# Performance work log

Measured on AMD Instinct MI355X. Metric: run time of the kernel, lower is better.

## Reference

```python
import jax, jax.numpy as jnp
import numpy as np

T = 4096          # total packed tokens (4 docs x 1024)
NUM_DOCS = 4
H = 16            # n_heads
D = 64            # head_dim == v_head_dim
TOPK = 64         # per-token top-k KV selection (<= min doc len)


def setup_inputs() -> dict:
    key = jax.random.key(0)
    kq, kk, kv, ki, ks = jax.random.split(key, 5)
    q = jax.random.normal(kq, (T, H, D), dtype=jnp.float32)
    k = jax.random.normal(kk, (T, H, D), dtype=jnp.float32)
    v = jax.random.normal(kv, (T, H, D), dtype=jnp.float32)
    # 4 equal-length documents of 1024 tokens
    cu_seqlens = (jnp.arange(NUM_DOCS + 1, dtype=jnp.int32) * (T // NUM_DOCS))
    # global top-k indices; reference clamps them into the owning document
    topk_indices = jax.random.randint(ki, (T, TOPK), 0, T, dtype=jnp.int32)
    # selector scores in (0,1), like indexer softmax outputs
    topk_scores = jax.random.uniform(ks, (T, TOPK), dtype=jnp.float32)
    return {
        "q_packed": q,
        "k_packed": k,
        "v_packed": v,
        "cu_seqlens": cu_seqlens,
        "topk_indices": topk_indices,
        "topk_scores": topk_scores,
    }


def reference(q_packed, k_packed, v_packed, cu_seqlens, topk_indices, topk_scores):
    total_tokens, n_heads, head_dim = q_packed.shape
    scale = head_dim ** -0.5

    # Per-token document assignment (vectorized replacement for the doc loop).
    tok = jnp.arange(total_tokens, dtype=cu_seqlens.dtype)
    seg = jnp.searchsorted(cu_seqlens[1:], tok, side="right")  # (T,) doc id
    start = cu_seqlens[seg]                                    # (T,)
    seq_len = cu_seqlens[seg + 1] - start                      # (T,)

    # Localize and clamp top-k indices into the owning document, then
    # convert back to global packed indices for gathering.
    local = jnp.clip(topk_indices - start[:, None], 0, (seq_len - 1)[:, None])
    gidx = start[:, None] + local                              # (T, K)

    k_gathered = k_packed[gidx]   # (T, K, H, D)
    v_gathered = v_packed[gidx]   # (T, K, H, D)

    # q . k_sel, softmax over the k selected keys
    scores = jnp.einsum("thd,tkhd->thk", q_packed, k_gathered) * scale
    w = jax.nn.softmax(scores, axis=-1)                        # (T, H, K)

    # Modulate by selector scores (head-shared) and renormalize.
    w = w * topk_scores[:, None, :]
    w = w / (jnp.sum(w, axis=-1, keepdims=True) + 1e-12)

    out = jnp.einsum("thk,tkhd->thd", w, v_gathered)           # (T, H, D)
    return out
```

## Files before the change

kernel.cpp:

```cpp
#include <hip/hip_runtime.h>
#include <hip/hip_fp16.h>


#define T_TOK 4096
#define NH    16
#define HD    64
#define KSEL  64
#define ROWS  (T_TOK * NH)

typedef _Float16 h2v __attribute__((ext_vector_type(2)));

static __device__ __forceinline__ h2v u2h2v(unsigned u) {
    return __builtin_bit_cast(h2v, u);
}
static __device__ __forceinline__ __half2 u2h2(unsigned u) {
    return __builtin_bit_cast(__half2, u);
}
static __device__ __forceinline__ h2v f2h2v(float a, float b) {
    __half2 t = __floats2half2_rn(a, b);
    return __builtin_bit_cast(h2v, t);
}
template<int CTRL>
static __device__ __forceinline__ float dpp_addf(float x) {
    const int s = __builtin_amdgcn_update_dpp(
        0, __builtin_bit_cast(int, x), CTRL, 0xF, 0xF, true);
    return x + __builtin_bit_cast(float, s);
}

__global__ __launch_bounds__(256) void cvt_kv(
    const float* __restrict__ kM, const float* __restrict__ vM,
    uint4* __restrict__ kvH)
{
    const int i  = blockIdx.x * blockDim.x + threadIdx.x;
    const int rh = i >> 4;
    const int c  = i & 15;
    const float4 fk = *(const float4*)(kM + rh * HD + c * 4);
    const float4 fv = *(const float4*)(vM + rh * HD + c * 4);
    uint4 o;
    o.x = __builtin_bit_cast(unsigned, __floats2half2_rn(fk.x, fk.y));
    o.y = __builtin_bit_cast(unsigned, __floats2half2_rn(fk.z, fk.w));
    o.z = __builtin_bit_cast(unsigned, __floats2half2_rn(fv.x, fv.y));
    o.w = __builtin_bit_cast(unsigned, __floats2half2_rn(fv.z, fv.w));
    kvH[i] = o;
}

__global__ __launch_bounds__(256) void dsa_sparse_attn(
    const float* __restrict__ qM,
    const uint4* __restrict__ kvH,
    const int*   __restrict__ cu,
    const int*   __restrict__ tidx,
    const float* __restrict__ tsc,
    float*       __restrict__ out,
    int num_docs)
{
    const int wave = threadIdx.x >> 6;
    const int lane = threadIdx.x & 63;

    const int b     = blockIdx.x;
    const int xcd   = b & 7;
    const int j     = b >> 3;
    const int tb    = j & 255;
    const int sw    = j >> 8;
    const int slice = xcd + (sw << 3);
    const int hg    = slice & 3;
    const int doc   = slice >> 2;
    const int h0    = hg << 2;
    const int t     = doc * (T_TOK / 4) + tb * 4 + wave;

    int seg = 0;
    for (int i = 1; i < num_docs; ++i)
        if (t >= cu[i]) seg = i;
    const int start = cu[seg];
    const int len   = cu[seg + 1] - start;

    int loc = tidx[t * KSEL + lane] - start;
    loc = loc < 0 ? 0 : (loc > len - 1 ? len - 1 : loc);
    const int g = start + loc;

    const int lh = lane >> 4;
    const int ld = lane & 15;

    const float4 qf = *(const float4*)(qM + (t * NH + h0 + lh) * HD + ld * 4);
    const h2v q01 = f2h2v(qf.x * 0.125f, qf.y * 0.125f);
    const h2v q23 = f2h2v(qf.z * 0.125f, qf.w * 0.125f);

    const float* scb = tsc + t * KSEL;

    float S2 = 0.f;
    __half2 acc0 = u2h2(0u), acc1 = u2h2(0u);

    #pragma unroll
    for (int r = 0; r < KSEL; ++r) {
        const int gr = __shfl(g, r, 64);
        const uint4 kv = kvH[((gr * NH + h0) << 4) + lane];
        float p = 0.f;
        p = __builtin_amdgcn_fdot2(u2h2v(kv.x), q01, p, false);
        p = __builtin_amdgcn_fdot2(u2h2v(kv.y), q23, p, false);
        p = dpp_addf<0xB1>(p);
        p = dpp_addf<0x4E>(p);
        p = dpp_addf<0x141>(p);
        p = dpp_addf<0x140>(p);
        const float w = __expf(p) * scb[r];
        S2 += w;
        const __half2 w2 = __floats2half2_rn(w, w);
        acc0 = __hfma2(w2, u2h2(kv.z), acc0);
        acc1 = __hfma2(w2, u2h2(kv.w), acc1);
    }

    const float inv = __builtin_amdgcn_rcpf(S2);
    const float2 a0 = __half22float2(acc0);
    const float2 a1 = __half22float2(acc1);
    *(float4*)(out + (t * NH + h0 + lh) * HD + ld * 4) =
        make_float4(a0.x * inv, a0.y * inv, a1.x * inv, a1.y * inv);
}

extern "C" void kernel_launch(void* const* d_in, const int* in_sizes, int n_in,
                              void* d_out, int out_size, void* d_ws, size_t ws_size,
                              hipStream_t stream) {
    const float* q   = (const float*)d_in[0];
    const float* k   = (const float*)d_in[1];
    const float* v   = (const float*)d_in[2];
    const int*   cu  = (const int*)d_in[3];
    const int*   ti  = (const int*)d_in[4];
    const float* ts  = (const float*)d_in[5];
    float*       out = (float*)d_out;
    const int num_docs = in_sizes[3] - 1;

    uint4* kvH = (uint4*)d_ws;

    hipLaunchKernelGGL(cvt_kv, dim3(ROWS * 16 / 256), dim3(256), 0, stream,
                       k, v, kvH);

    hipLaunchKernelGGL(dsa_sparse_attn, dim3(4096), dim3(256), 0, stream,
                       q, kvH, cu, ti, ts, out, num_docs);
}
```

Measured before the change: 141.2 us.

## Software-pipeline KV gathers with four independent accumulators and exp2 scaling

Replaces the simple unrolled loop with a compile-time recursive stage that issues the next four KV gathers before processing the current four, and splits the softmax sum and output accumulators into four independent chains. It folds log2(e) into the query scale so the raw hardware v_exp_f32 replaces __expf. It also precomputes the gather base offset per lane and loads selector scores once per lane, broadcasting them with a shuffle instead of a scalar load per iteration. The aim is to hide gather latency and shorten dependency chains, at the cost of more live registers and small changes in fp16 rounding.

```diff
diff --git a/kernel.cpp b/kernel.cpp
--- a/kernel.cpp
+++ b/kernel.cpp
@@ -26,6 +26,11 @@
         0, __builtin_bit_cast(int, x), CTRL, 0xF, 0xF, true);
     return x + __builtin_bit_cast(float, s);
 }
+static __device__ __forceinline__ float exp2_hw(float x) {
+    float r;
+    asm("v_exp_f32 %0, %1" : "=v"(r) : "v"(x));
+    return r;
+}
 
 __global__ __launch_bounds__(256) void cvt_kv(
     const float* __restrict__ kM, const float* __restrict__ vM,
@@ -42,6 +47,55 @@
     o.z = __builtin_bit_cast(unsigned, __floats2half2_rn(fv.x, fv.y));
     o.w = __builtin_bit_cast(unsigned, __floats2half2_rn(fv.z, fv.w));
     kvH[i] = o;
+}
+
+struct PState {
+    h2v q01, q23;
+    float scl;
+    int gbase, lane;
+    float s0, s1, s2, s3;
+    __half2 a00, a01, a10, a11, a20, a21, a30, a31;
+    const uint4* __restrict__ kvH;
+};
+
+template<int RR>
+static __device__ __forceinline__ uint4 loadkv(const PState& st) {
+    return st.kvH[(unsigned)__shfl(st.gbase, RR, 64) + st.lane];
+}
+
+template<int RR>
+static __device__ __forceinline__ void proc(PState& st, const uint4 kv,
+                                            float& SA, __half2& A0, __half2& A1) {
+    float p = __builtin_amdgcn_fdot2(u2h2v(kv.x), st.q01, 0.f, false);
+    p = __builtin_amdgcn_fdot2(u2h2v(kv.y), st.q23, p, false);
+    p = dpp_addf<0xB1>(p);
+    p = dpp_addf<0x4E>(p);
+    p = dpp_addf<0x141>(p);
+    p = dpp_addf<0x140>(p);
+    const float w = exp2_hw(p) * __shfl(st.scl, RR, 64);
+    SA += w;
+    const __half2 w2 = __floats2half2_rn(w, w);
+    A0 = __hfma2(w2, u2h2(kv.z), A0);
+    A1 = __hfma2(w2, u2h2(kv.w), A1);
+}
+
+template<int R>
+static __device__ __forceinline__ void stage(PState& st, uint4 kv0, uint4 kv1,
+                                             uint4 kv2, uint4 kv3) {
+    if constexpr (R + 4 < KSEL) {
+        uint4 n0 = loadkv<R + 4>(st), n1 = loadkv<R + 5>(st),
+              n2 = loadkv<R + 6>(st), n3 = loadkv<R + 7>(st);
+        proc<R + 0>(st, kv0, st.s0, st.a00, st.a01);
+        proc<R + 1>(st, kv1, st.s1, st.a10, st.a11);
+        proc<R + 2>(st, kv2, st.s2, st.a20, st.a21);
+        proc<R + 3>(st, kv3, st.s3, st.a30, st.a31);
+        stage<R + 4>(st, n0, n1, n2, n3);
+    } else {
+        proc<R + 0>(st, kv0, st.s0, st.a00, st.a01);
+        proc<R + 1>(st, kv1, st.s1, st.a10, st.a11);
+        proc<R + 2>(st, kv2, st.s2, st.a20, st.a21);
+        proc<R + 3>(st, kv3, st.s3, st.a30, st.a31);
+    }
 }
 
 __global__ __launch_bounds__(256) void dsa_sparse_attn(
@@ -80,38 +134,33 @@
     const int lh = lane >> 4;
     const int ld = lane & 15;
 
+    const float qs = 0.125f * 1.44269504088896f;
     const float4 qf = *(const float4*)(qM + (t * NH + h0 + lh) * HD + ld * 4);
-    const h2v q01 = f2h2v(qf.x * 0.125f, qf.y * 0.125f);
-    const h2v q23 = f2h2v(qf.z * 0.125f, qf.w * 0.125f);
 
-    const float* scb = tsc + t * KSEL;
+    PState st;
+    st.q01 = f2h2v(qf.x * qs, qf.y * qs);
+    st.q23 = f2h2v(qf.z * qs, qf.w * qs);
+    st.scl = tsc[t * KSEL + lane];
+    st.gbase = (g * NH + h0) << 4;
+    st.lane = lane;
+    st.kvH = kvH;
+    st.s0 = st.s1 = st.s2 = st.s3 = 0.f;
+    st.a00 = st.a01 = st.a10 = st.a11 = u2h2(0u);
+    st.a20 = st.a21 = st.a30 = st.a31 = u2h2(0u);
 
-    float S2 = 0.f;
-    __half2 acc0 = u2h2(0u), acc1 = u2h2(0u);
+    uint4 kv0 = loadkv<0>(st), kv1 = loadkv<1>(st),
+          kv2 = loadkv<2>(st), kv3 = loadkv<3>(st);
+    stage<0>(st, kv0, kv1, kv2, kv3);
 
-    #pragma unroll
-    for (int r = 0; r < KSEL; ++r) {
-        const int gr = __shfl(g, r, 64);
-        const uint4 kv = kvH[((gr * NH + h0) << 4) + lane];
-        float p = 0.f;
-        p = __builtin_amdgcn_fdot2(u2h2v(kv.x), q01, p, false);
-        p = __builtin_amdgcn_fdot2(u2h2v(kv.y), q23, p, false);
-        p = dpp_addf<0xB1>(p);
-        p = dpp_addf<0x4E>(p);
-        p = dpp_addf<0x141>(p);
-        p = dpp_addf<0x140>(p);
-        const float w = __expf(p) * scb[r];
-        S2 += w;
-        const __half2 w2 = __floats2half2_rn(w, w);
-        acc0 = __hfma2(w2, u2h2(kv.z), acc0);
-        acc1 = __hfma2(w2, u2h2(kv.w), acc1);
-    }
+    const float S2 = (st.s0 + st.s1) + (st.s2 + st.s3);
+    const float inv = __builtin_amdgcn_rcpf(S2);
+    const __half2 acc0 = __hadd2(__hadd2(st.a00, st.a10), __hadd2(st.a20, st.a30));
+    const __half2 acc1 = __hadd2(__hadd2(st.a01, st.a11), __hadd2(st.a21, st.a31));
 
-    const float inv = __builtin_amdgcn_rcpf(S2);
-    const float2 a0 = __half22float2(acc0);
-    const float2 a1 = __half22float2(acc1);
+    const float2 f0 = __half22float2(acc0);
+    const float2 f1 = __half22float2(acc1);
     *(float4*)(out + (t * NH + h0 + lh) * HD + ld * 4) =
-        make_float4(a0.x * inv, a0.y * inv, a1.x * inv, a1.y * inv);
+        make_float4(f0.x * inv, f0.y * inv, f1.x * inv, f1.y * inv);
 }
 
 extern "C" void kernel_launch(void* const* d_in, const int* in_sizes, int n_in,
```

New measurement: 140.0 us. No clear change (-0.9%).

## Stage per-head KV document slices in LDS and bucket top-k entries per stage

Applied to the files above, without the earlier changes.

Relayouts the fp16 KV workspace head-major, then assigns each block one (doc, head) pair and 64 tokens. Each block streams the document's KV rows for that head through shared memory in 8 stages, and uses ballot/mbcnt to compact each token's selected indices that fall in the current stage into an LDS entry list. Softmax is computed with exp2 and a pre-folded log2e scale, using two accumulator sets. This replaces random global gathers with coalesced staged loads and LDS reuse across tokens. In exchange it adds many barriers, assumes the document structure maps onto chunks of 64 tokens, and relies on fixed stage sizing (SROWS 128 rows per stage).

```diff
diff --git a/kernel.cpp b/kernel.cpp
--- a/kernel.cpp
+++ b/kernel.cpp
@@ -7,6 +7,9 @@
 #define HD    64
 #define KSEL  64
 #define ROWS  (T_TOK * NH)
+#define CHTOK 64
+#define NSTG  8
+#define SROWS 128
 
 typedef _Float16 h2v __attribute__((ext_vector_type(2)));
 
@@ -26,25 +29,33 @@
         0, __builtin_bit_cast(int, x), CTRL, 0xF, 0xF, true);
     return x + __builtin_bit_cast(float, s);
 }
+static __device__ __forceinline__ float exp2_hw(float x) {
+    float r;
+    asm("v_exp_f32 %0, %1" : "=v"(r) : "v"(x));
+    return r;
+}
 
 __global__ __launch_bounds__(256) void cvt_kv(
     const float* __restrict__ kM, const float* __restrict__ vM,
     uint4* __restrict__ kvH)
 {
-    const int i  = blockIdx.x * blockDim.x + threadIdx.x;
-    const int rh = i >> 4;
-    const int c  = i & 15;
-    const float4 fk = *(const float4*)(kM + rh * HD + c * 4);
-    const float4 fv = *(const float4*)(vM + rh * HD + c * 4);
+    const int i = blockIdx.x * blockDim.x + threadIdx.x;
+    const int c = i & 15;
+    const int g = (i >> 4) & (T_TOK - 1);
+    const int h = i >> 16;
+    const int rh = g * NH + h;
+    const float* src = (c < 8 ? kM : vM) + rh * HD + (c & 7) * 8;
+    const float4 f0 = *(const float4*)(src);
+    const float4 f1 = *(const float4*)(src + 4);
     uint4 o;
-    o.x = __builtin_bit_cast(unsigned, __floats2half2_rn(fk.x, fk.y));
-    o.y = __builtin_bit_cast(unsigned, __floats2half2_rn(fk.z, fk.w));
-    o.z = __builtin_bit_cast(unsigned, __floats2half2_rn(fv.x, fv.y));
-    o.w = __builtin_bit_cast(unsigned, __floats2half2_rn(fv.z, fv.w));
+    o.x = __builtin_bit_cast(unsigned, __floats2half2_rn(f0.x, f0.y));
+    o.y = __builtin_bit_cast(unsigned, __floats2half2_rn(f0.z, f0.w));
+    o.z = __builtin_bit_cast(unsigned, __floats2half2_rn(f1.x, f1.y));
+    o.w = __builtin_bit_cast(unsigned, __floats2half2_rn(f1.z, f1.w));
     kvH[i] = o;
 }
 
-__global__ __launch_bounds__(256) void dsa_sparse_attn(
+__global__ __launch_bounds__(512, 6) void dsa_sparse_attn(
     const float* __restrict__ qM,
     const uint4* __restrict__ kvH,
     const int*   __restrict__ cu,
@@ -53,65 +64,148 @@
     float*       __restrict__ out,
     int num_docs)
 {
-    const int wave = threadIdx.x >> 6;
-    const int lane = threadIdx.x & 63;
+    (void)num_docs;
+    __shared__ uint4    kvb[SROWS * 16];
+    __shared__ unsigned ent[CHTOK * KSEL];
+
+    const int tid  = threadIdx.x;
+    const int wave = tid >> 6;
+    const int lane = tid & 63;
+    const int grp  = lane >> 3;
+    const int l8   = lane & 7;
 
     const int b     = blockIdx.x;
     const int xcd   = b & 7;
-    const int j     = b >> 3;
-    const int tb    = j & 255;
-    const int sw    = j >> 8;
-    const int slice = xcd + (sw << 3);
-    const int hg    = slice & 3;
-    const int doc   = slice >> 2;
-    const int h0    = hg << 2;
-    const int t     = doc * (T_TOK / 4) + tb * 4 + wave;
-
-    int seg = 0;
-    for (int i = 1; i < num_docs; ++i)
-        if (t >= cu[i]) seg = i;
-    const int start = cu[seg];
-    const int len   = cu[seg + 1] - start;
-
-    int loc = tidx[t * KSEL + lane] - start;
-    loc = loc < 0 ? 0 : (loc > len - 1 ? len - 1 : loc);
-    const int g = start + loc;
-
-    const int lh = lane >> 4;
-    const int ld = lane & 15;
-
-    const float4 qf = *(const float4*)(qM + (t * NH + h0 + lh) * HD + ld * 4);
-    const h2v q01 = f2h2v(qf.x * 0.125f, qf.y * 0.125f);
-    const h2v q23 = f2h2v(qf.z * 0.125f, qf.w * 0.125f);
-
-    const float* scb = tsc + t * KSEL;
-
-    float S2 = 0.f;
-    __half2 acc0 = u2h2(0u), acc1 = u2h2(0u);
-
+    const int idx   = b >> 3;
+    const int pair  = xcd * 8 + (idx & 7);
+    const int chunk = idx >> 3;
+    const int doc   = pair >> 4;
+    const int head  = pair & 15;
+
+    const int start = cu[doc];
+    const int len   = cu[doc + 1] - start;
+
+    const int tokslot = wave * 8 + grp;
+    const int t = start + chunk * CHTOK + tokslot;
+
+    const float qs = 0.125f * 1.44269504088896f;
+    const float* qp = qM + (t * NH + head) * HD + l8 * 8;
+    const float4 qa = *(const float4*)qp;
+    const float4 qb = *(const float4*)(qp + 4);
+    const h2v q0 = f2h2v(qa.x * qs, qa.y * qs);
+    const h2v q1 = f2h2v(qa.z * qs, qa.w * qs);
+    const h2v q2 = f2h2v(qb.x * qs, qb.y * qs);
+    const h2v q3 = f2h2v(qb.z * qs, qb.w * qs);
+
+    const int4 ia = *(const int4*)(tidx + t * KSEL + l8 * 8);
+    const int4 ib = *(const int4*)(tidx + t * KSEL + l8 * 8 + 4);
+    const uint4 sa = *(const uint4*)(tsc + t * KSEL + l8 * 8);
+    const uint4 sb = *(const uint4*)(tsc + t * KSEL + l8 * 8 + 4);
+
+    int g[8];
+    unsigned sbits[8];
+    g[0]=ia.x; g[1]=ia.y; g[2]=ia.z; g[3]=ia.w;
+    g[4]=ib.x; g[5]=ib.y; g[6]=ib.z; g[7]=ib.w;
+    sbits[0]=sa.x; sbits[1]=sa.y; sbits[2]=sa.z; sbits[3]=sa.w;
+    sbits[4]=sb.x; sbits[5]=sb.y; sbits[6]=sb.z; sbits[7]=sb.w;
     #pragma unroll
-    for (int r = 0; r < KSEL; ++r) {
-        const int gr = __shfl(g, r, 64);
-        const uint4 kv = kvH[((gr * NH + h0) << 4) + lane];
-        float p = 0.f;
-        p = __builtin_amdgcn_fdot2(u2h2v(kv.x), q01, p, false);
-        p = __builtin_amdgcn_fdot2(u2h2v(kv.y), q23, p, false);
-        p = dpp_addf<0xB1>(p);
-        p = dpp_addf<0x4E>(p);
-        p = dpp_addf<0x141>(p);
-        p = dpp_addf<0x140>(p);
-        const float w = __expf(p) * scb[r];
-        S2 += w;
-        const __half2 w2 = __floats2half2_rn(w, w);
-        acc0 = __hfma2(w2, u2h2(kv.z), acc0);
-        acc1 = __hfma2(w2, u2h2(kv.w), acc1);
+    for (int j = 0; j < 8; ++j) {
+        int loc = g[j] - start;
+        loc = loc < 0 ? 0 : (loc > len - 1 ? len - 1 : loc);
+        g[j] = start + loc;
     }
 
-    const float inv = __builtin_amdgcn_rcpf(S2);
-    const float2 a0 = __half22float2(acc0);
-    const float2 a1 = __half22float2(acc1);
-    *(float4*)(out + (t * NH + h0 + lh) * HD + ld * 4) =
-        make_float4(a0.x * inv, a0.y * inv, a1.x * inv, a1.y * inv);
+    const unsigned sh  = (grp & 3) * 8;
+    const unsigned mlo = (grp < 4) ? (0xFFu << sh) : 0u;
+    const unsigned mhi = (grp < 4) ? 0u : (0xFFu << sh);
+
+    float S0 = 0.f, S1 = 0.f;
+    __half2 a00 = u2h2(0u), a01 = u2h2(0u), a02 = u2h2(0u), a03 = u2h2(0u);
+    __half2 a10 = u2h2(0u), a11 = u2h2(0u), a12 = u2h2(0u), a13 = u2h2(0u);
+
+#define BODY(I, SS, A0, A1, A2, A3) {                                      \
+    const unsigned e_ = ent[(tokslot << 6) | (((I) + tokslot) & 63)];      \
+    const float sc_ = __builtin_bit_cast(float, e_ << 8);                  \
+    const int lr_ = (int)(e_ >> 24);                                       \
+    const uint4 kk_ = kvb[lr_ * 16 + l8];                                  \
+    const uint4 vv_ = kvb[lr_ * 16 + 8 + l8];                              \
+    float p_ = __builtin_amdgcn_fdot2(u2h2v(kk_.x), q0, 0.f, false);       \
+    p_ = __builtin_amdgcn_fdot2(u2h2v(kk_.y), q1, p_, false);              \
+    p_ = __builtin_amdgcn_fdot2(u2h2v(kk_.z), q2, p_, false);              \
+    p_ = __builtin_amdgcn_fdot2(u2h2v(kk_.w), q3, p_, false);              \
+    p_ = dpp_addf<0xB1>(p_);                                               \
+    p_ = dpp_addf<0x4E>(p_);                                               \
+    p_ = dpp_addf<0x141>(p_);                                              \
+    const float w_ = exp2_hw(p_) * sc_;                                    \
+    SS += w_;                                                              \
+    const __half2 w2_ = __floats2half2_rn(w_, w_);                         \
+    A0 = __hfma2(w2_, u2h2(vv_.x), A0);                                    \
+    A1 = __hfma2(w2_, u2h2(vv_.y), A1);                                    \
+    A2 = __hfma2(w2_, u2h2(vv_.z), A2);                                    \
+    A3 = __hfma2(w2_, u2h2(vv_.w), A3);                                    \
+}
+
+    for (int e = 0; e < NSTG; ++e) {
+        const int elo  = (len * e) >> 3;
+        const int qn   = ((len * (e + 1)) >> 3) - elo;
+        const int grow = start + elo;
+        const uint4* src = kvH + (size_t)(head * T_TOK + grow) * 16;
+        const int lim = qn * 16;
+
+        uint4 st0, st1, st2, st3;
+        if (tid < lim)        st0 = src[tid];
+        if (tid + 512 < lim)  st1 = src[tid + 512];
+        if (tid + 1024 < lim) st2 = src[tid + 1024];
+        if (tid + 1536 < lim) st3 = src[tid + 1536];
+
+        unsigned cbase = 0;
+        #pragma unroll
+        for (int j = 0; j < 8; ++j) {
+            const int lr = g[j] - grow;
+            const bool pr = (unsigned)lr < (unsigned)qn;
+            const unsigned long long bal = __ballot(pr);
+            const unsigned blo = (unsigned)bal & mlo;
+            const unsigned bhi = (unsigned)(bal >> 32) & mhi;
+            const unsigned rank = __builtin_amdgcn_mbcnt_hi(
+                bhi, __builtin_amdgcn_mbcnt_lo(blo, 0));
+            if (pr) {
+                const unsigned pos = (cbase + rank + (unsigned)tokslot) & 63u;
+                ent[(tokslot << 6) | pos] =
+                    ((unsigned)lr << 24) | (sbits[j] >> 8);
+            }
+            cbase += (unsigned)(__popc(blo) + __popc(bhi));
+        }
+        const int n = (int)cbase;
+
+        __syncthreads();
+        if (tid < lim)        kvb[tid] = st0;
+        if (tid + 512 < lim)  kvb[tid + 512] = st1;
+        if (tid + 1024 < lim) kvb[tid + 1024] = st2;
+        if (tid + 1536 < lim) kvb[tid + 1536] = st3;
+        __syncthreads();
+
+        int i = 0;
+        for (; i + 1 < n; i += 2) {
+            BODY(i,     S0, a00, a01, a02, a03);
+            BODY(i + 1, S1, a10, a11, a12, a13);
+        }
+        if (i < n) BODY(i, S0, a00, a01, a02, a03);
+    }
+#undef BODY
+
+    const float S   = S0 + S1;
+    const float inv = __builtin_amdgcn_rcpf(S);
+    const __half2 b0 = __hadd2(a00, a10);
+    const __half2 b1 = __hadd2(a01, a11);
+    const __half2 b2 = __hadd2(a02, a12);
+    const __half2 b3 = __hadd2(a03, a13);
+    const float2 f0 = __half22float2(b0);
+    const float2 f1 = __half22float2(b1);
+    const float2 f2 = __half22float2(b2);
+    const float2 f3 = __half22float2(b3);
+    float* op = out + (t * NH + head) * HD + l8 * 8;
+    *(float4*)op       = make_float4(f0.x * inv, f0.y * inv, f1.x * inv, f1.y * inv);
+    *(float4*)(op + 4) = make_float4(f2.x * inv, f2.y * inv, f3.x * inv, f3.y * inv);
 }
 
 extern "C" void kernel_launch(void* const* d_in, const int* in_sizes, int n_in,
@@ -131,6 +225,6 @@
     hipLaunchKernelGGL(cvt_kv, dim3(ROWS * 16 / 256), dim3(256), 0, stream,
                        k, v, kvH);
 
-    hipLaunchKernelGGL(dsa_sparse_attn, dim3(4096), dim3(256), 0, stream,
+    hipLaunchKernelGGL(dsa_sparse_attn, dim3(1024), dim3(512), 0, stream,
                        q, kvH, cu, ti, ts, out, num_docs);
 }
```

New measurement: 156.8 us. +11.1%, slower.

## Replace sparse gather attention with dense per-document MFMA attention using a selector-weight matrix

Applied to the files above, without the earlier changes.

Rewrites the sparse top-k attention as dense attention within each document. Selector scores are scattered into a per-token dense weight row over the document, with duplicate indices summed. The main kernel then runs Q·K^T and P·V with f16 MFMA over all 1024 keys per document, using a transposed V and an LDS double stage. This removes the random per-key gathers and replaces them with dense tensor-core work, at the cost of about 16x more FLOPs and an extra preprocessing pass. It relies on selection within a document, clamps exponents without max subtraction, and hardcodes 4 equal documents of 1024 tokens with tiles of 256 tokens.

```diff
diff --git a/kernel.cpp b/kernel.cpp
--- a/kernel.cpp
+++ b/kernel.cpp
@@ -6,19 +6,15 @@
 #define NH    16
 #define HD    64
 #define KSEL  64
-#define ROWS  (T_TOK * NH)
-
-typedef _Float16 h2v __attribute__((ext_vector_type(2)));
-
-static __device__ __forceinline__ h2v u2h2v(unsigned u) {
-    return __builtin_bit_cast(h2v, u);
-}
-static __device__ __forceinline__ __half2 u2h2(unsigned u) {
-    return __builtin_bit_cast(__half2, u);
-}
-static __device__ __forceinline__ h2v f2h2v(float a, float b) {
-    __half2 t = __floats2half2_rn(a, b);
-    return __builtin_bit_cast(h2v, t);
+
+typedef _Float16 f16;
+typedef _Float16 f16x8 __attribute__((ext_vector_type(8)));
+typedef float    f32x4 __attribute__((ext_vector_type(4)));
+
+#define LSTR 72
+
+static __device__ __forceinline__ float exp2_hw(float x) {
+    float r; asm("v_exp_f32 %0, %1" : "=v"(r) : "v"(x)); return r;
 }
 template<int CTRL>
 static __device__ __forceinline__ float dpp_addf(float x) {
@@ -26,92 +22,236 @@
         0, __builtin_bit_cast(int, x), CTRL, 0xF, 0xF, true);
     return x + __builtin_bit_cast(float, s);
 }
-
-__global__ __launch_bounds__(256) void cvt_kv(
-    const float* __restrict__ kM, const float* __restrict__ vM,
-    uint4* __restrict__ kvH)
+static __device__ __forceinline__ uint4 pack8(float4 a, float4 b) {
+    uint4 u;
+    u.x = __builtin_bit_cast(unsigned, __floats2half2_rn(a.x, a.y));
+    u.y = __builtin_bit_cast(unsigned, __floats2half2_rn(a.z, a.w));
+    u.z = __builtin_bit_cast(unsigned, __floats2half2_rn(b.x, b.y));
+    u.w = __builtin_bit_cast(unsigned, __floats2half2_rn(b.z, b.w));
+    return u;
+}
+
+__global__ __launch_bounds__(256) void vt_build(
+    const float* __restrict__ vM, uint4* __restrict__ vT)
 {
-    const int i  = blockIdx.x * blockDim.x + threadIdx.x;
-    const int rh = i >> 4;
-    const int c  = i & 15;
-    const float4 fk = *(const float4*)(kM + rh * HD + c * 4);
-    const float4 fv = *(const float4*)(vM + rh * HD + c * 4);
-    uint4 o;
-    o.x = __builtin_bit_cast(unsigned, __floats2half2_rn(fk.x, fk.y));
-    o.y = __builtin_bit_cast(unsigned, __floats2half2_rn(fk.z, fk.w));
-    o.z = __builtin_bit_cast(unsigned, __floats2half2_rn(fv.x, fv.y));
-    o.w = __builtin_bit_cast(unsigned, __floats2half2_rn(fv.z, fv.w));
-    kvH[i] = o;
-}
-
-__global__ __launch_bounds__(256) void dsa_sparse_attn(
-    const float* __restrict__ qM,
-    const uint4* __restrict__ kvH,
-    const int*   __restrict__ cu,
-    const int*   __restrict__ tidx,
-    const float* __restrict__ tsc,
-    float*       __restrict__ out,
-    int num_docs)
+    __shared__ __align__(16) f16 T[64 * 136];
+    const int h  = blockIdx.x >> 5;
+    const int gb = blockIdx.x & 31;
+    const int tid = threadIdx.x;
+    const int gl = tid >> 1, hf = tid & 1;
+    const float* src = vM + (((gb * 128 + gl) * NH + h) << 6) + 32 * hf;
+    #pragma unroll
+    for (int jj = 0; jj < 8; ++jj) {
+        const float4 f = *(const float4*)(src + 4 * jj);
+        const int d0 = 32 * hf + 4 * jj;
+        T[(d0 + 0) * 136 + gl] = (f16)f.x;
+        T[(d0 + 1) * 136 + gl] = (f16)f.y;
+        T[(d0 + 2) * 136 + gl] = (f16)f.z;
+        T[(d0 + 3) * 136 + gl] = (f16)f.w;
+    }
+    __syncthreads();
+    #pragma unroll
+    for (int k = 0; k < 4; ++k) {
+        const int idx = tid + 256 * k;
+        const int d = idx >> 4, c = idx & 15;
+        vT[((h * HD + d) << 9) + (gb << 4) + c] = *(const uint4*)&T[d * 136 + 8 * c];
+    }
+}
+
+__global__ __launch_bounds__(256) void sel_build(
+    const int* __restrict__ tidx, const float* __restrict__ tsc,
+    const int* __restrict__ cu, uint4* __restrict__ selH, int num_docs)
 {
-    const int wave = threadIdx.x >> 6;
-    const int lane = threadIdx.x & 63;
-
-    const int b     = blockIdx.x;
-    const int xcd   = b & 7;
-    const int j     = b >> 3;
-    const int tb    = j & 255;
-    const int sw    = j >> 8;
-    const int slice = xcd + (sw << 3);
-    const int hg    = slice & 3;
-    const int doc   = slice >> 2;
-    const int h0    = hg << 2;
-    const int t     = doc * (T_TOK / 4) + tb * 4 + wave;
-
+    __shared__ float row[4][1024];
+    const int wv = threadIdx.x >> 6, l = threadIdx.x & 63;
+    const int t = blockIdx.x * 4 + wv;
+    #pragma unroll
+    for (int k = 0; k < 4; ++k)
+        *(float4*)&row[wv][l * 16 + 4 * k] = make_float4(0.f, 0.f, 0.f, 0.f);
+    __syncthreads();
     int seg = 0;
-    for (int i = 1; i < num_docs; ++i)
-        if (t >= cu[i]) seg = i;
+    for (int i = 1; i < num_docs; ++i) if (t >= cu[i]) seg = i;
     const int start = cu[seg];
     const int len   = cu[seg + 1] - start;
-
-    int loc = tidx[t * KSEL + lane] - start;
+    int loc = tidx[t * KSEL + l] - start;
     loc = loc < 0 ? 0 : (loc > len - 1 ? len - 1 : loc);
-    const int g = start + loc;
-
-    const int lh = lane >> 4;
-    const int ld = lane & 15;
-
-    const float4 qf = *(const float4*)(qM + (t * NH + h0 + lh) * HD + ld * 4);
-    const h2v q01 = f2h2v(qf.x * 0.125f, qf.y * 0.125f);
-    const h2v q23 = f2h2v(qf.z * 0.125f, qf.w * 0.125f);
-
-    const float* scb = tsc + t * KSEL;
-
-    float S2 = 0.f;
-    __half2 acc0 = u2h2(0u), acc1 = u2h2(0u);
-
-    #pragma unroll
-    for (int r = 0; r < KSEL; ++r) {
-        const int gr = __shfl(g, r, 64);
-        const uint4 kv = kvH[((gr * NH + h0) << 4) + lane];
-        float p = 0.f;
-        p = __builtin_amdgcn_fdot2(u2h2v(kv.x), q01, p, false);
-        p = __builtin_amdgcn_fdot2(u2h2v(kv.y), q23, p, false);
-        p = dpp_addf<0xB1>(p);
-        p = dpp_addf<0x4E>(p);
-        p = dpp_addf<0x141>(p);
-        p = dpp_addf<0x140>(p);
-        const float w = __expf(p) * scb[r];
-        S2 += w;
-        const __half2 w2 = __floats2half2_rn(w, w);
-        acc0 = __hfma2(w2, u2h2(kv.z), acc0);
-        acc1 = __hfma2(w2, u2h2(kv.w), acc1);
-    }
-
-    const float inv = __builtin_amdgcn_rcpf(S2);
-    const float2 a0 = __half22float2(acc0);
-    const float2 a1 = __half22float2(acc1);
-    *(float4*)(out + (t * NH + h0 + lh) * HD + ld * 4) =
-        make_float4(a0.x * inv, a0.y * inv, a1.x * inv, a1.y * inv);
+    atomicAdd(&row[wv][loc], tsc[t * KSEL + l]);
+    __syncthreads();
+    #pragma unroll
+    for (int k = 0; k < 2; ++k) {
+        const float* rp = &row[wv][l * 16 + 8 * k];
+        const float4 a = *(const float4*)rp;
+        const float4 b = *(const float4*)(rp + 4);
+        selH[(t << 7) + l * 2 + k] = pack8(a, b);
+    }
+}
+
+__global__ __launch_bounds__(512, 2) void dsa_main(
+    const float* __restrict__ qM,
+    const float* __restrict__ kM,
+    const uint4* __restrict__ vT,
+    const uint4* __restrict__ selH,
+    const int*   __restrict__ cu,
+    float*       __restrict__ out)
+{
+    __shared__ __align__(16) f16 KtS[64 * LSTR];
+    __shared__ __align__(16) f16 VtS[64 * LSTR];
+    __shared__ __align__(16) f16 PS[256 * LSTR];
+
+    const int tid = threadIdx.x;
+    const int w   = tid >> 6;
+    const int l   = tid & 63;
+    const int g4  = l >> 4;
+    const int c16 = l & 15;
+
+    const int b    = blockIdx.x;
+    const int head = ((b & 7) << 1) | ((b >> 3) & 1);
+    const int doc  = (b >> 4) & 3;
+    const int qt   = b >> 6;
+
+    const int start = cu[doc];
+    const int len   = cu[doc + 1] - start;
+    const int t0    = start + qt * 256;
+
+    const float qs = 0.125f * 1.44269504088896f;
+    f16x8 qf[2][2];
+    #pragma unroll
+    for (int m = 0; m < 2; ++m)
+    #pragma unroll
+    for (int ks = 0; ks < 2; ++ks) {
+        const float* qp = qM + (((t0 + 32 * w + 16 * m + c16) * NH + head) << 6)
+                        + 32 * ks + 8 * g4;
+        float4 a = *(const float4*)qp;
+        float4 c = *(const float4*)(qp + 4);
+        a.x *= qs; a.y *= qs; a.z *= qs; a.w *= qs;
+        c.x *= qs; c.y *= qs; c.z *= qs; c.w *= qs;
+        qf[m][ks] = __builtin_bit_cast(f16x8, pack8(a, c));
+    }
+
+    f32x4 O[2][4];
+    float psum[2][4];
+    #pragma unroll
+    for (int m = 0; m < 2; ++m)
+    #pragma unroll
+    for (int sd = 0; sd < 4; ++sd) {
+        O[m][sd] = (f32x4){0.f, 0.f, 0.f, 0.f};
+        psum[m][sd] = 0.f;
+    }
+
+    const int NT = (len + 63) >> 6;
+    const int r8 = tid >> 3, c8 = tid & 7;
+
+    uint4 kq, vq, sq0, sq1, sq2, sq3;
+#define LOADSTAGE(IT) {                                                     \
+        const int grow_ = start + (IT) * 64;                                \
+        const float* kp_ = kM + (((grow_ + r8) * NH + head) << 6) + 8 * c8; \
+        const float4 ka_ = *(const float4*)kp_;                             \
+        const float4 kb_ = *(const float4*)(kp_ + 4);                       \
+        kq  = pack8(ka_, kb_);                                              \
+        vq  = vT[((head * HD + r8) << 9) + (grow_ >> 3) + c8];              \
+        sq0 = selH[((t0 + r8      ) << 7) + ((IT) << 3) + c8];              \
+        sq1 = selH[((t0 + r8 +  64) << 7) + ((IT) << 3) + c8];              \
+        sq2 = selH[((t0 + r8 + 128) << 7) + ((IT) << 3) + c8];              \
+        sq3 = selH[((t0 + r8 + 192) << 7) + ((IT) << 3) + c8];              \
+    }
+#define WRITESTAGE() {                                                      \
+        ((uint4*)KtS)[r8 * 9 + c8] = kq;                                    \
+        ((uint4*)VtS)[r8 * 9 + c8] = vq;                                    \
+        ((uint4*)PS)[(r8      ) * 9 + c8] = sq0;                            \
+        ((uint4*)PS)[(r8 +  64) * 9 + c8] = sq1;                            \
+        ((uint4*)PS)[(r8 + 128) * 9 + c8] = sq2;                            \
+        ((uint4*)PS)[(r8 + 192) * 9 + c8] = sq3;                            \
+    }
+
+    LOADSTAGE(0);
+    WRITESTAGE();
+    __syncthreads();
+
+    for (int it = 0; it < NT; ++it) {
+        const bool more = (it + 1 < NT);
+        if (more) LOADSTAGE(it + 1);
+
+        f32x4 S[2][4];
+        #pragma unroll
+        for (int m = 0; m < 2; ++m)
+        #pragma unroll
+        for (int s = 0; s < 4; ++s)
+            S[m][s] = (f32x4){0.f, 0.f, 0.f, 0.f};
+        #pragma unroll
+        for (int ks = 0; ks < 2; ++ks) {
+            f16x8 kf[4];
+            #pragma unroll
+            for (int s = 0; s < 4; ++s)
+                kf[s] = __builtin_bit_cast(f16x8,
+                    ((const uint4*)KtS)[(16 * s + c16) * 9 + 4 * ks + g4]);
+            #pragma unroll
+            for (int m = 0; m < 2; ++m)
+            #pragma unroll
+            for (int s = 0; s < 4; ++s)
+                S[m][s] = __builtin_amdgcn_mfma_f32_16x16x32_f16(
+                    qf[m][ks], kf[s], S[m][s], 0, 0, 0);
+        }
+
+        #pragma unroll
+        for (int m = 0; m < 2; ++m)
+        #pragma unroll
+        for (int s = 0; s < 4; ++s)
+        #pragma unroll
+        for (int r = 0; r < 4; ++r) {
+            const int tok  = 32 * w + 16 * m + 4 * g4 + r;
+            const int hidx = tok * LSTR + 16 * s + c16;
+            const float sel = (float)PS[hidx];
+            const float p = fminf(exp2_hw(fminf(S[m][s][r], 30.f)) * sel,
+                                  60000.f);
+            psum[m][r] += p;
+            PS[hidx] = (f16)p;
+        }
+
+        __syncthreads();
+
+        #pragma unroll
+        for (int ks = 0; ks < 2; ++ks) {
+            f16x8 af[2];
+            #pragma unroll
+            for (int m = 0; m < 2; ++m)
+                af[m] = __builtin_bit_cast(f16x8,
+                    ((const uint4*)PS)[(32 * w + 16 * m + c16) * 9 + 4 * ks + g4]);
+            #pragma unroll
+            for (int sd = 0; sd < 4; ++sd) {
+                const f16x8 vf = __builtin_bit_cast(f16x8,
+                    ((const uint4*)VtS)[(16 * sd + c16) * 9 + 4 * ks + g4]);
+                #pragma unroll
+                for (int m = 0; m < 2; ++m)
+                    O[m][sd] = __builtin_amdgcn_mfma_f32_16x16x32_f16(
+                        af[m], vf, O[m][sd], 0, 0, 0);
+            }
+        }
+
+        if (more) {
+            __syncthreads();
+            WRITESTAGE();
+            __syncthreads();
+        }
+    }
+#undef LOADSTAGE
+#undef WRITESTAGE
+
+    #pragma unroll
+    for (int m = 0; m < 2; ++m)
+    #pragma unroll
+    for (int r = 0; r < 4; ++r) {
+        float sum = psum[m][r];
+        sum = dpp_addf<0xB1>(sum);
+        sum = dpp_addf<0x4E>(sum);
+        sum = dpp_addf<0x141>(sum);
+        sum = dpp_addf<0x140>(sum);
+        const float inv = __builtin_amdgcn_rcpf(sum);
+        const int t = t0 + 32 * w + 16 * m + 4 * g4 + r;
+        float* op = out + ((t * NH + head) << 6) + c16;
+        #pragma unroll
+        for (int sd = 0; sd < 4; ++sd)
+            op[16 * sd] = O[m][sd][r] * inv;
+    }
 }
 
 extern "C" void kernel_launch(void* const* d_in, const int* in_sizes, int n_in,
@@ -126,11 +266,12 @@
     float*       out = (float*)d_out;
     const int num_docs = in_sizes[3] - 1;
 
-    uint4* kvH = (uint4*)d_ws;
-
-    hipLaunchKernelGGL(cvt_kv, dim3(ROWS * 16 / 256), dim3(256), 0, stream,
-                       k, v, kvH);
-
-    hipLaunchKernelGGL(dsa_sparse_attn, dim3(4096), dim3(256), 0, stream,
-                       q, kvH, cu, ti, ts, out, num_docs);
-}
+    uint4* vTp = (uint4*)d_ws;
+    uint4* sH  = (uint4*)((char*)d_ws + (size_t)8 * 1024 * 1024);
+
+    hipLaunchKernelGGL(vt_build,  dim3(512),  dim3(256), 0, stream, v, vTp);
+    hipLaunchKernelGGL(sel_build, dim3(1024), dim3(256), 0, stream,
+                       ti, ts, cu, sH, num_docs);
+    hipLaunchKernelGGL(dsa_main,  dim3(256),  dim3(512), 0, stream,
+                       q, k, vTp, sH, cu, out);
+}
```

After: 151.4 us. 7.2% more time.
